# Kernel optimization log

Measured on AMD Instinct MI355X. Metric: run time of the kernel, lower is better.

Reference implementation:

```python
import jax, jax.numpy as jnp
import numpy as np
import math

B, L, N, DIM, H = 2, 8, 1024, 512, 8
DH = DIM // H

def setup_inputs() -> dict:
    key = jax.random.key(0)
    ks = jax.random.split(key, 9)
    s = 1.0 / math.sqrt(DIM)
    return {
        "x": jax.random.normal(ks[0], (B, L, N, DIM), dtype=jnp.float32),
        "Wq": jax.random.normal(ks[1], (DIM, DIM), dtype=jnp.float32) * s,
        "bq": jnp.zeros((DIM,), dtype=jnp.float32),
        "Wk": jax.random.normal(ks[2], (DIM, DIM), dtype=jnp.float32) * s,
        "bk": jnp.zeros((DIM,), dtype=jnp.float32),
        "Wv": jax.random.normal(ks[3], (DIM, DIM), dtype=jnp.float32) * s,
        "bv": jnp.zeros((DIM,), dtype=jnp.float32),
        "Wo": jax.random.normal(ks[4], (DIM, DIM), dtype=jnp.float32) * s,
        "bo": jnp.zeros((DIM,), dtype=jnp.float32),
    }

def _split_heads(t):
    # 'b l n (h d) -> b l h n d'
    b, l, n, _ = t.shape
    return t.reshape(b, l, n, H, DH).transpose(0, 1, 3, 2, 4)

def reference(x, Wq, bq, Wk, bk, Wv, bv, Wo, bo):
    q = _split_heads(x @ Wq.T + bq)
    # FAITHFUL BUG: source maps (q, v, k) -> (q_mat, k_mat, v_mat),
    # so the "keys" come from the v projection and "values" from the k projection.
    k_mat = _split_heads(x @ Wv.T + bv)
    v_mat = _split_heads(x @ Wk.T + bk)
    # scale is sqrt(Dh * num_heads) = sqrt(dim), as in the source
    scores = jnp.einsum('blhnd,blhmd->blhnm', q, k_mat) / math.sqrt(DIM)
    weights = jax.nn.softmax(scores, axis=-1)
    inter = jnp.einsum('blhnm,blhmd->blhnd', weights, v_mat)
    # 'b l h n d -> b l n (h d)'
    inter = inter.transpose(0, 1, 3, 2, 4).reshape(x.shape[0], x.shape[1], x.shape[2], DIM)
    return inter @ Wo.T + bo
```

## Files before the change

kernel.cpp:

```cpp
#include <hip/hip_runtime.h>
#include <stdint.h>

#define DIMC 512
#define NSEQ 1024
#define BLT  16
#define NHEAD 8
#define DHD  64
#define MTOT (BLT*NSEQ)

typedef float f32x4 __attribute__((ext_vector_type(4)));
typedef short s16x8 __attribute__((ext_vector_type(8)));
typedef short s16x4 __attribute__((ext_vector_type(4)));

__device__ __forceinline__ unsigned short f2bf(float f) {
    unsigned int u = __float_as_uint(f);
    u += 0x7fffu + ((u >> 16) & 1u);
    return (unsigned short)(u >> 16);
}
__device__ __forceinline__ float bf2f(unsigned short h) {
    return __uint_as_float(((unsigned int)h) << 16);
}

#define QSCALE (0.04419417382415922f * 1.4426950408889634f)

__device__ __forceinline__ void gll16(const void* g, void* l) {
    __builtin_amdgcn_global_load_lds(
        (const __attribute__((address_space(1))) void*)g,
        (__attribute__((address_space(3))) void*)l, 16, 0, 0);
}

__device__ __forceinline__ f32x4 mfma16_bf16(s16x4 a, s16x4 b, f32x4 c) {
#if __has_builtin(__builtin_amdgcn_mfma_f32_16x16x16bf16_1k)
    return __builtin_amdgcn_mfma_f32_16x16x16bf16_1k(a, b, c, 0, 0, 0);
#else
    asm volatile("v_mfma_f32_16x16x16_bf16 %0, %1, %2, %0"
                 : "+v"(c) : "v"(a), "v"(b));
    return c;
#endif
}

__device__ __forceinline__ bool detect_bf16(const unsigned short* x) {
    int t = threadIdx.x & 63;
    unsigned short v = x[2 * t];
    int e = (v >> 7) & 0xFF;
    unsigned long long ball = __ballot(e < 100 || e > 137);
    return __popcll(ball) < 16;
}

struct ConvArgs {
    const void* src[9];
    unsigned short* dst[9];
};

__global__ __launch_bounds__(256) void conv_kernel(ConvArgs a,
                                                   const unsigned short* __restrict__ xdet) {
    const bool isbf = detect_bf16(xdet);
    int b = blockIdx.x;
    int seg, idx;
    if (b < 4096)      { seg = 0; idx = (b * 256 + threadIdx.x) * 8; }
    else if (b < 4608) { int t = b - 4096; seg = 1 + (t >> 7);
                         idx = (((t & 127) * 256) + threadIdx.x) * 8; }
    else               { int i = threadIdx.x * 8; seg = 5 + (i >> 9); idx = i & 511; }
    const void* s = a.src[seg];
    unsigned short* d = a.dst[seg];
    if (isbf) {
        *(uint4*)(d + idx) = *(const uint4*)((const unsigned short*)s + idx);
    } else {
        float4 t0 = *(const float4*)((const float*)s + idx);
        float4 t1 = *(const float4*)((const float*)s + idx + 4);
        ushort4 v0{f2bf(t0.x), f2bf(t0.y), f2bf(t0.z), f2bf(t0.w)};
        ushort4 v1{f2bf(t1.x), f2bf(t1.y), f2bf(t1.z), f2bf(t1.w)};
        *(ushort4*)(d + idx)     = v0;
        *(ushort4*)(d + idx + 4) = v1;
    }
}

__device__ __forceinline__ void gemm_core_async(
    const unsigned short* __restrict__ Ap, const unsigned short* __restrict__ Wp,
    int mBase, int nBase, unsigned short* Al, unsigned short* Bl, f32x4 acc[4][4])
{
    const int wave = threadIdx.x >> 6;
    const int lane = threadIdx.x & 63;
    const int lr = lane & 15, lg = lane >> 4;
    const int wm = wave >> 1, wn = wave & 1;
    const int srow = lane >> 3;
    const int scol = (lane & 7) * 8;

    #pragma unroll
    for (int a = 0; a < 4; ++a)
        #pragma unroll
        for (int b = 0; b < 4; ++b) acc[a][b] = (f32x4){0.f, 0.f, 0.f, 0.f};

    for (int k0 = 0; k0 < DIMC; k0 += 64) {
        #pragma unroll
        for (int i = 0; i < 4; ++i) {
            int rbase = (wave * 4 + i) * 8;
            gll16(Ap + (long)(mBase + rbase + srow) * DIMC + k0 + scol, Al + rbase * 64);
            gll16(Wp + (long)(nBase + rbase + srow) * DIMC + k0 + scol, Bl + rbase * 64);
        }
        __syncthreads();

        #pragma unroll
        for (int kk = 0; kk < 64; kk += 32) {
            s16x8 af[4], bf_[4];
            #pragma unroll
            for (int a = 0; a < 4; ++a)
                af[a] = *(const s16x8*)&Al[(wm * 64 + a * 16 + lr) * 64 + kk + lg * 8];
            #pragma unroll
            for (int b = 0; b < 4; ++b)
                bf_[b] = *(const s16x8*)&Bl[(wn * 64 + b * 16 + lr) * 64 + kk + lg * 8];
            #pragma unroll
            for (int a = 0; a < 4; ++a)
                #pragma unroll
                for (int b = 0; b < 4; ++b)
                    acc[a][b] = __builtin_amdgcn_mfma_f32_16x16x32_bf16(af[a], bf_[b], acc[a][b], 0, 0, 0);
        }
        __syncthreads();
    }
}

__global__ __launch_bounds__(256) void proj_kernel(
    const unsigned short* __restrict__ xb,
    const unsigned short* __restrict__ Wqb, const unsigned short* __restrict__ Wkb,
    const unsigned short* __restrict__ Wvb,
    const unsigned short* __restrict__ bqb, const unsigned short* __restrict__ bkb,
    const unsigned short* __restrict__ bvb,
    unsigned short* __restrict__ Q, unsigned short* __restrict__ K,
    unsigned short* __restrict__ Vt)
{
    const int z = blockIdx.z;
    const unsigned short* Wp = (z == 0) ? Wqb : ((z == 1) ? Wvb : Wkb);
    const unsigned short* bp = (z == 0) ? bqb : ((z == 1) ? bvb : bkb);
    unsigned short* outp = (z == 0) ? Q : ((z == 1) ? K : Vt);
    const float oscale = (z == 0) ? QSCALE : 1.0f;

    const int mBase = blockIdx.x * 128;
    const int nBase = blockIdx.y * 128;
    const int lane = threadIdx.x & 63;
    const int lr = lane & 15, lg = lane >> 4;
    const int wm = (threadIdx.x >> 6) >> 1, wn = (threadIdx.x >> 6) & 1;

    __shared__ unsigned short Al[128 * 64];
    __shared__ unsigned short Bl[128 * 64];
    f32x4 acc[4][4];
    gemm_core_async(xb, Wp, mBase, nBase, Al, Bl, acc);

    #pragma unroll
    for (int b = 0; b < 4; ++b) {
        int j = nBase + wn * 64 + b * 16 + lr;
        float bb = bf2f(bp[j]);
        int h = j >> 6, d = j & 63;
        #pragma unroll
        for (int a = 0; a < 4; ++a) {
            int m0 = mBase + wm * 64 + a * 16 + lg * 4;
            int bl = m0 >> 10, n0 = m0 & 1023;
            if (z == 2) {
                ushort4 pk;
                unsigned short* p = (unsigned short*)&pk;
                #pragma unroll
                for (int r = 0; r < 4; ++r) p[r] = f2bf(acc[a][b][r] + bb);
                *(ushort4*)&outp[(((bl << 3) + h) << 16) + (d << 10) + n0] = pk;
            } else {
                #pragma unroll
                for (int r = 0; r < 4; ++r) {
                    float v = (acc[a][b][r] + bb) * oscale;
                    outp[(((bl << 3) + h) << 16) + ((n0 + r) << 6) + d] = f2bf(v);
                }
            }
        }
    }
}

__global__ __launch_bounds__(256) void out_gemm_kernel(
    const unsigned short* __restrict__ inter, const unsigned short* __restrict__ Wob,
    const unsigned short* __restrict__ bob, void* __restrict__ outp,
    const unsigned short* __restrict__ xdet)
{
    const bool isbf = detect_bf16(xdet);
    const int mBase = blockIdx.x * 128;
    const int nBase = blockIdx.y * 128;
    const int lane = threadIdx.x & 63;
    const int lr = lane & 15, lg = lane >> 4;
    const int wm = (threadIdx.x >> 6) >> 1, wn = (threadIdx.x >> 6) & 1;

    __shared__ unsigned short Al[128 * 64];
    __shared__ unsigned short Bl[128 * 64];
    f32x4 acc[4][4];
    gemm_core_async(inter, Wob, mBase, nBase, Al, Bl, acc);

    #pragma unroll
    for (int b = 0; b < 4; ++b) {
        int j = nBase + wn * 64 + b * 16 + lr;
        float bb = bf2f(bob[j]);
        #pragma unroll
        for (int a = 0; a < 4; ++a) {
            #pragma unroll
            for (int r = 0; r < 4; ++r) {
                long m = mBase + wm * 64 + a * 16 + lg * 4 + r;
                float v = acc[a][b][r] + bb;
                if (isbf) ((unsigned short*)outp)[m * DIMC + j] = f2bf(v);
                else      ((float*)outp)[m * DIMC + j] = v;
            }
        }
    }
}

#define SWZ(row, col) ((row) * 64 + ((col) ^ (((row) & 7) * 8)))

__global__ __launch_bounds__(256, 3) void attn_kernel(
    const unsigned short* __restrict__ Q, const unsigned short* __restrict__ K,
    const unsigned short* __restrict__ Vt, unsigned short* __restrict__ inter)
{
    const int b = blockIdx.x;
    const int bh = b & 127;
    const int qt = b >> 7;
    const int wave = threadIdx.x >> 6;
    const int lane = threadIdx.x & 63;
    const int lr = lane & 15;
    const int lg = lane >> 4;

    const unsigned short* Qb = Q + (long)bh * (NSEQ * DHD);
    const int qbase = qt * 128 + wave * 32;

    s16x8 qf[2][2];
    #pragma unroll
    for (int g = 0; g < 2; ++g)
        #pragma unroll
        for (int kk = 0; kk < 2; ++kk)
            qf[g][kk] = *(const s16x8*)&Qb[(qbase + g * 16 + lr) * DHD + kk * 32 + lg * 8];

    __shared__ unsigned short Kl[64 * 64];
    __shared__ unsigned short Vl[64 * 64];

    f32x4 o[2][4];
    #pragma unroll
    for (int g = 0; g < 2; ++g)
        #pragma unroll
        for (int m = 0; m < 4; ++m) o[g][m] = (f32x4){0.f, 0.f, 0.f, 0.f};
    float l_acc[2] = {0.f, 0.f};

    for (int kt = 0; kt < 16; ++kt) {
        const unsigned short* Kb = K + (long)bh * (NSEQ * DHD) + kt * 64 * DHD;
        const unsigned short* Vb = Vt + (long)bh * (NSEQ * DHD) + kt * 64;

        #pragma unroll
        for (int i = 0; i < 2; ++i) {
            int f = threadIdx.x + 256 * i;
            int row = f >> 3, c8 = (f & 7) * 8;
            *(uint4*)&Kl[SWZ(row, c8)] = *(const uint4*)&Kb[row * DHD + c8];
            *(uint4*)&Vl[SWZ(row, c8)] = *(const uint4*)&Vb[row * NSEQ + c8];
        }
        __syncthreads();

        f32x4 s[2][4];
        #pragma unroll
        for (int g = 0; g < 2; ++g)
            #pragma unroll
            for (int c = 0; c < 4; ++c) s[g][c] = (f32x4){0.f, 0.f, 0.f, 0.f};
        #pragma unroll
        for (int kk = 0; kk < 2; ++kk) {
            s16x8 af[4];
            #pragma unroll
            for (int c = 0; c < 4; ++c)
                af[c] = *(const s16x8*)&Kl[SWZ(c * 16 + lr, kk * 32 + lg * 8)];
            #pragma unroll
            for (int g = 0; g < 2; ++g)
                #pragma unroll
                for (int c = 0; c < 4; ++c)
                    s[g][c] = __builtin_amdgcn_mfma_f32_16x16x32_bf16(af[c], qf[g][kk], s[g][c], 0, 0, 0);
        }

        s16x4 pb[2][4];
        #pragma unroll
        for (int g = 0; g < 2; ++g)
            #pragma unroll
            for (int c = 0; c < 4; ++c) {
                float p0 = __builtin_exp2f(s[g][c][0]);
                float p1 = __builtin_exp2f(s[g][c][1]);
                float p2 = __builtin_exp2f(s[g][c][2]);
                float p3 = __builtin_exp2f(s[g][c][3]);
                l_acc[g] += (p0 + p1) + (p2 + p3);
                unsigned int u0 = __float_as_uint(p0) + 0x8000u;
                unsigned int u1 = __float_as_uint(p1) + 0x8000u;
                unsigned int u2 = __float_as_uint(p2) + 0x8000u;
                unsigned int u3 = __float_as_uint(p3) + 0x8000u;
                union { s16x4 v; unsigned int u[2]; } pk;
                pk.u[0] = __builtin_amdgcn_perm(u1, u0, 0x07060302u);
                pk.u[1] = __builtin_amdgcn_perm(u3, u2, 0x07060302u);
                pb[g][c] = pk.v;
            }

        #pragma unroll
        for (int c = 0; c < 4; ++c) {
            s16x4 va[4];
            #pragma unroll
            for (int m = 0; m < 4; ++m)
                va[m] = *(const s16x4*)&Vl[SWZ(m * 16 + lr, c * 16 + lg * 4)];
            #pragma unroll
            for (int g = 0; g < 2; ++g)
                #pragma unroll
                for (int m = 0; m < 4; ++m)
                    o[g][m] = mfma16_bf16(va[m], pb[g][c], o[g][m]);
        }
        __syncthreads();
    }

    const int bl = bh >> 3, h = bh & 7;
    #pragma unroll
    for (int g = 0; g < 2; ++g) {
        float l = l_acc[g];
        l += __shfl_xor(l, 16);
        l += __shfl_xor(l, 32);
        float inv = 1.f / l;
        const int n = qbase + g * 16 + lr;
        #pragma unroll
        for (int m = 0; m < 4; ++m) {
            ushort4 pk;
            unsigned short* p = (unsigned short*)&pk;
            #pragma unroll
            for (int r = 0; r < 4; ++r) p[r] = f2bf(o[g][m][r] * inv);
            *(ushort4*)&inter[((long)(bl * NSEQ + n)) * DIMC + h * 64 + m * 16 + lg * 4] = pk;
        }
    }
}

extern "C" void kernel_launch(void* const* d_in, const int* in_sizes, int n_in,
                              void* d_out, int out_size, void* d_ws, size_t ws_size,
                              hipStream_t stream) {
    const void* x  = d_in[0];
    const void* Wq = d_in[1]; const void* bq = d_in[2];
    const void* Wk = d_in[3]; const void* bk = d_in[4];
    const void* Wv = d_in[5]; const void* bv = d_in[6];
    const void* Wo = d_in[7]; const void* bo = d_in[8];

    char* ws = (char*)d_ws;
    unsigned short* xb  = (unsigned short*)ws;
    unsigned short* Q   = xb + (long)MTOT * DIMC;
    unsigned short* K   = Q  + (long)MTOT * DIMC;
    unsigned short* Vt  = K  + (long)MTOT * DIMC;
    unsigned short* Wqb = Vt + (long)MTOT * DIMC;
    unsigned short* Wkb = Wqb + DIMC * DIMC;
    unsigned short* Wvb = Wkb + DIMC * DIMC;
    unsigned short* Wob = Wvb + DIMC * DIMC;
    unsigned short* bqb = Wob + DIMC * DIMC;
    unsigned short* bkb = bqb + DIMC;
    unsigned short* bvb = bkb + DIMC;
    unsigned short* bob = bvb + DIMC;

    ConvArgs ca;
    ca.src[0] = x;  ca.src[1] = Wq; ca.src[2] = Wk; ca.src[3] = Wv; ca.src[4] = Wo;
    ca.src[5] = bq; ca.src[6] = bk; ca.src[7] = bv; ca.src[8] = bo;
    ca.dst[0] = xb;  ca.dst[1] = Wqb; ca.dst[2] = Wkb; ca.dst[3] = Wvb; ca.dst[4] = Wob;
    ca.dst[5] = bqb; ca.dst[6] = bkb; ca.dst[7] = bvb; ca.dst[8] = bob;
    conv_kernel<<<4609, 256, 0, stream>>>(ca, (const unsigned short*)x);

    dim3 gp(MTOT / 128, DIMC / 128, 3);
    proj_kernel<<<gp, 256, 0, stream>>>(xb, Wqb, Wkb, Wvb, bqb, bkb, bvb, Q, K, Vt);

    attn_kernel<<<8 * 128, 256, 0, stream>>>(Q, K, Vt, xb );

    dim3 go(MTOT / 128, DIMC / 128);
    out_gemm_kernel<<<go, 256, 0, stream>>>(xb , Wob, bob, d_out,
                                            (const unsigned short*)x);
}
```

Before: 224.1 us.

## Fuse x fp32-to-bf16 conversion into projection GEMM and double-buffer attention K/V

Removes the separate conversion pass over x by letting the projection GEMM load fp32 rows directly, convert them in registers and store bf16 into LDS. Only the weights and biases still go through the conversion kernel. The attention kernel now double-buffers K/V tiles in LDS, prefetching the next tile into registers while computing on the current one, and its launch-bounds occupancy hint rises from 3 to 4. The trade-offs are that each projection block re-reads and re-converts x (three z slices × four n tiles), the fp32 path uses synchronous loads instead of async global-to-LDS copies, and the attention kernel uses more LDS and registers.

```diff
diff --git a/kernel.cpp b/kernel.cpp
--- a/kernel.cpp
+++ b/kernel.cpp
@@ -52,15 +52,13 @@
     unsigned short* dst[9];
 };
 
-__global__ __launch_bounds__(256) void conv_kernel(ConvArgs a,
-                                                   const unsigned short* __restrict__ xdet) {
+__global__ __launch_bounds__(256) void wconv_kernel(ConvArgs a,
+                                                    const unsigned short* __restrict__ xdet) {
     const bool isbf = detect_bf16(xdet);
     int b = blockIdx.x;
     int seg, idx;
-    if (b < 4096)      { seg = 0; idx = (b * 256 + threadIdx.x) * 8; }
-    else if (b < 4608) { int t = b - 4096; seg = 1 + (t >> 7);
-                         idx = (((t & 127) * 256) + threadIdx.x) * 8; }
-    else               { int i = threadIdx.x * 8; seg = 5 + (i >> 9); idx = i & 511; }
+    if (b < 512) { seg = 1 + (b >> 7); idx = ((b & 127) * 256 + threadIdx.x) * 8; }
+    else         { int i = threadIdx.x * 8; seg = 5 + (i >> 9); idx = i & 511; }
     const void* s = a.src[seg];
     unsigned short* d = a.dst[seg];
     if (isbf) {
@@ -75,8 +73,8 @@
     }
 }
 
-__device__ __forceinline__ void gemm_core_async(
-    const unsigned short* __restrict__ Ap, const unsigned short* __restrict__ Wp,
+__device__ __forceinline__ void gemm_core_mixed(
+    const void* __restrict__ Ap, bool aBf, const unsigned short* __restrict__ Wp,
     int mBase, int nBase, unsigned short* Al, unsigned short* Bl, f32x4 acc[4][4])
 {
     const int wave = threadIdx.x >> 6;
@@ -92,10 +90,26 @@
         for (int b = 0; b < 4; ++b) acc[a][b] = (f32x4){0.f, 0.f, 0.f, 0.f};
 
     for (int k0 = 0; k0 < DIMC; k0 += 64) {
+        if (aBf) {
+            #pragma unroll
+            for (int i = 0; i < 4; ++i) {
+                int rbase = (wave * 4 + i) * 8;
+                gll16((const unsigned short*)Ap + (long)(mBase + rbase + srow) * DIMC + k0 + scol,
+                      Al + rbase * 64);
+            }
+        } else {
+            #pragma unroll
+            for (int i = 0; i < 8; ++i) {
+                int q = threadIdx.x + 256 * i;
+                int row = q >> 4, c4 = (q & 15) * 4;
+                float4 t = *(const float4*)((const float*)Ap + (long)(mBase + row) * DIMC + k0 + c4);
+                ushort4 v{f2bf(t.x), f2bf(t.y), f2bf(t.z), f2bf(t.w)};
+                *(ushort4*)&Al[row * 64 + c4] = v;
+            }
+        }
         #pragma unroll
         for (int i = 0; i < 4; ++i) {
             int rbase = (wave * 4 + i) * 8;
-            gll16(Ap + (long)(mBase + rbase + srow) * DIMC + k0 + scol, Al + rbase * 64);
             gll16(Wp + (long)(nBase + rbase + srow) * DIMC + k0 + scol, Bl + rbase * 64);
         }
         __syncthreads();
@@ -120,7 +134,7 @@
 }
 
 __global__ __launch_bounds__(256) void proj_kernel(
-    const unsigned short* __restrict__ xb,
+    const void* __restrict__ xp,
     const unsigned short* __restrict__ Wqb, const unsigned short* __restrict__ Wkb,
     const unsigned short* __restrict__ Wvb,
     const unsigned short* __restrict__ bqb, const unsigned short* __restrict__ bkb,
@@ -128,6 +142,7 @@
     unsigned short* __restrict__ Q, unsigned short* __restrict__ K,
     unsigned short* __restrict__ Vt)
 {
+    const bool isbf = detect_bf16((const unsigned short*)xp);
     const int z = blockIdx.z;
     const unsigned short* Wp = (z == 0) ? Wqb : ((z == 1) ? Wvb : Wkb);
     const unsigned short* bp = (z == 0) ? bqb : ((z == 1) ? bvb : bkb);
@@ -143,7 +158,7 @@
     __shared__ unsigned short Al[128 * 64];
     __shared__ unsigned short Bl[128 * 64];
     f32x4 acc[4][4];
-    gemm_core_async(xb, Wp, mBase, nBase, Al, Bl, acc);
+    gemm_core_mixed(xp, isbf, Wp, mBase, nBase, Al, Bl, acc);
 
     #pragma unroll
     for (int b = 0; b < 4; ++b) {
@@ -186,7 +201,7 @@
     __shared__ unsigned short Al[128 * 64];
     __shared__ unsigned short Bl[128 * 64];
     f32x4 acc[4][4];
-    gemm_core_async(inter, Wob, mBase, nBase, Al, Bl, acc);
+    gemm_core_mixed(inter, true, Wob, mBase, nBase, Al, Bl, acc);
 
     #pragma unroll
     for (int b = 0; b < 4; ++b) {
@@ -207,7 +222,7 @@
 
 #define SWZ(row, col) ((row) * 64 + ((col) ^ (((row) & 7) * 8)))
 
-__global__ __launch_bounds__(256, 3) void attn_kernel(
+__global__ __launch_bounds__(256, 4) void attn_kernel(
     const unsigned short* __restrict__ Q, const unsigned short* __restrict__ K,
     const unsigned short* __restrict__ Vt, unsigned short* __restrict__ inter)
 {
@@ -220,6 +235,8 @@
     const int lg = lane >> 4;
 
     const unsigned short* Qb = Q + (long)bh * (NSEQ * DHD);
+    const unsigned short* Kb0 = K + (long)bh * (NSEQ * DHD);
+    const unsigned short* Vb0 = Vt + (long)bh * (NSEQ * DHD);
     const int qbase = qt * 128 + wave * 32;
 
     s16x8 qf[2][2];
@@ -229,8 +246,23 @@
         for (int kk = 0; kk < 2; ++kk)
             qf[g][kk] = *(const s16x8*)&Qb[(qbase + g * 16 + lr) * DHD + kk * 32 + lg * 8];
 
-    __shared__ unsigned short Kl[64 * 64];
-    __shared__ unsigned short Vl[64 * 64];
+    __shared__ unsigned short Kl[2][64 * 64];
+    __shared__ unsigned short Vl[2][64 * 64];
+
+    const int f0 = threadIdx.x,      row0 = f0 >> 3, c80 = (f0 & 7) * 8;
+    const int f1 = threadIdx.x + 256, row1 = f1 >> 3, c81 = (f1 & 7) * 8;
+
+    {
+        uint4 ka = *(const uint4*)&Kb0[row0 * DHD + c80];
+        uint4 kb = *(const uint4*)&Kb0[row1 * DHD + c81];
+        uint4 va = *(const uint4*)&Vb0[row0 * NSEQ + c80];
+        uint4 vb = *(const uint4*)&Vb0[row1 * NSEQ + c81];
+        *(uint4*)&Kl[0][SWZ(row0, c80)] = ka;
+        *(uint4*)&Kl[0][SWZ(row1, c81)] = kb;
+        *(uint4*)&Vl[0][SWZ(row0, c80)] = va;
+        *(uint4*)&Vl[0][SWZ(row1, c81)] = vb;
+    }
+    __syncthreads();
 
     f32x4 o[2][4];
     #pragma unroll
@@ -240,17 +272,17 @@
     float l_acc[2] = {0.f, 0.f};
 
     for (int kt = 0; kt < 16; ++kt) {
-        const unsigned short* Kb = K + (long)bh * (NSEQ * DHD) + kt * 64 * DHD;
-        const unsigned short* Vb = Vt + (long)bh * (NSEQ * DHD) + kt * 64;
-
-        #pragma unroll
-        for (int i = 0; i < 2; ++i) {
-            int f = threadIdx.x + 256 * i;
-            int row = f >> 3, c8 = (f & 7) * 8;
-            *(uint4*)&Kl[SWZ(row, c8)] = *(const uint4*)&Kb[row * DHD + c8];
-            *(uint4*)&Vl[SWZ(row, c8)] = *(const uint4*)&Vb[row * NSEQ + c8];
-        }
-        __syncthreads();
+        const int cur = kt & 1, nxt = cur ^ 1;
+
+        uint4 ka, kb, va, vb;
+        if (kt < 15) {
+            const unsigned short* Kb = Kb0 + (kt + 1) * 64 * DHD;
+            const unsigned short* Vb = Vb0 + (kt + 1) * 64;
+            ka = *(const uint4*)&Kb[row0 * DHD + c80];
+            kb = *(const uint4*)&Kb[row1 * DHD + c81];
+            va = *(const uint4*)&Vb[row0 * NSEQ + c80];
+            vb = *(const uint4*)&Vb[row1 * NSEQ + c81];
+        }
 
         f32x4 s[2][4];
         #pragma unroll
@@ -262,7 +294,7 @@
             s16x8 af[4];
             #pragma unroll
             for (int c = 0; c < 4; ++c)
-                af[c] = *(const s16x8*)&Kl[SWZ(c * 16 + lr, kk * 32 + lg * 8)];
+                af[c] = *(const s16x8*)&Kl[cur][SWZ(c * 16 + lr, kk * 32 + lg * 8)];
             #pragma unroll
             for (int g = 0; g < 2; ++g)
                 #pragma unroll
@@ -292,15 +324,22 @@
 
         #pragma unroll
         for (int c = 0; c < 4; ++c) {
-            s16x4 va[4];
+            s16x4 va_[4];
             #pragma unroll
             for (int m = 0; m < 4; ++m)
-                va[m] = *(const s16x4*)&Vl[SWZ(m * 16 + lr, c * 16 + lg * 4)];
+                va_[m] = *(const s16x4*)&Vl[cur][SWZ(m * 16 + lr, c * 16 + lg * 4)];
             #pragma unroll
             for (int g = 0; g < 2; ++g)
                 #pragma unroll
                 for (int m = 0; m < 4; ++m)
-                    o[g][m] = mfma16_bf16(va[m], pb[g][c], o[g][m]);
+                    o[g][m] = mfma16_bf16(va_[m], pb[g][c], o[g][m]);
+        }
+
+        if (kt < 15) {
+            *(uint4*)&Kl[nxt][SWZ(row0, c80)] = ka;
+            *(uint4*)&Kl[nxt][SWZ(row1, c81)] = kb;
+            *(uint4*)&Vl[nxt][SWZ(row0, c80)] = va;
+            *(uint4*)&Vl[nxt][SWZ(row1, c81)] = vb;
         }
         __syncthreads();
     }
@@ -334,8 +373,8 @@
     const void* Wo = d_in[7]; const void* bo = d_in[8];
 
     char* ws = (char*)d_ws;
-    unsigned short* xb  = (unsigned short*)ws;
-    unsigned short* Q   = xb + (long)MTOT * DIMC;
+    unsigned short* inter = (unsigned short*)ws;
+    unsigned short* Q   = inter + (long)MTOT * DIMC;
     unsigned short* K   = Q  + (long)MTOT * DIMC;
     unsigned short* Vt  = K  + (long)MTOT * DIMC;
     unsigned short* Wqb = Vt + (long)MTOT * DIMC;
@@ -350,16 +389,16 @@
     ConvArgs ca;
     ca.src[0] = x;  ca.src[1] = Wq; ca.src[2] = Wk; ca.src[3] = Wv; ca.src[4] = Wo;
     ca.src[5] = bq; ca.src[6] = bk; ca.src[7] = bv; ca.src[8] = bo;
-    ca.dst[0] = xb;  ca.dst[1] = Wqb; ca.dst[2] = Wkb; ca.dst[3] = Wvb; ca.dst[4] = Wob;
+    ca.dst[0] = nullptr; ca.dst[1] = Wqb; ca.dst[2] = Wkb; ca.dst[3] = Wvb; ca.dst[4] = Wob;
     ca.dst[5] = bqb; ca.dst[6] = bkb; ca.dst[7] = bvb; ca.dst[8] = bob;
-    conv_kernel<<<4609, 256, 0, stream>>>(ca, (const unsigned short*)x);
+    wconv_kernel<<<513, 256, 0, stream>>>(ca, (const unsigned short*)x);
 
     dim3 gp(MTOT / 128, DIMC / 128, 3);
-    proj_kernel<<<gp, 256, 0, stream>>>(xb, Wqb, Wkb, Wvb, bqb, bkb, bvb, Q, K, Vt);
-
-    attn_kernel<<<8 * 128, 256, 0, stream>>>(Q, K, Vt, xb );
+    proj_kernel<<<gp, 256, 0, stream>>>(x, Wqb, Wkb, Wvb, bqb, bkb, bvb, Q, K, Vt);
+
+    attn_kernel<<<8 * 128, 256, 0, stream>>>(Q, K, Vt, inter);
 
     dim3 go(MTOT / 128, DIMC / 128);
-    out_gemm_kernel<<<go, 256, 0, stream>>>(xb , Wob, bob, d_out,
+    out_gemm_kernel<<<go, 256, 0, stream>>>(inter, Wob, bob, d_out,
                                             (const unsigned short*)x);
 }
```

Result: slower. 235.5 us (+5.1%).
